# Performance work log

Hardware: AMD Instinct MI355X
Metric: run time of the kernel (lower is better)

## Reference

```python
import jax, jax.numpy as jnp
import numpy as np

# conv_ada hyperparameters from init_kwargs: ka=1, alpha=0.25, kw=0.2
KA1 = 1.0          # activation scale for conv1 (ka)
KA2 = 1.25         # activation scale for conv2 (ka + alpha)
KW = 0.2           # weight clipping threshold used by the binary weight STE


def ste_sign(x, clip=1.0):
    """Binary sign with straight-through estimator (hardtanh-style clip).
    Forward value is sign(x); gradient is that of clip(x, -clip, clip)."""
    xc = jnp.clip(x, -clip, clip)
    return xc + jax.lax.stop_gradient(jnp.sign(x) - xc)


def conv_bin(x, w, ka, kw):
    """1-bit activation / 1-bit weight 3x3 conv (conv_ada).
    Activations -> ka * sign(x); weights -> per-out-channel mean(|w|) * sign(w)."""
    xq = ka * ste_sign(x)
    alpha_w = jnp.mean(jnp.abs(w), axis=(1, 2, 3), keepdims=True)  # [O,1,1,1]
    wq = alpha_w * ste_sign(w, kw)
    return jax.lax.conv_general_dilated(
        xq, wq, window_strides=(1, 1), padding='SAME',
        dimension_numbers=('NCHW', 'OIHW', 'NCHW'))


def prelu(x, slope):
    # per-channel PReLU, slope shape [C]
    return jnp.where(x >= 0, x, slope[None, :, None, None] * x)


def pixel_shuffle(x, r=2):
    b, c, h, w = x.shape
    co = c // (r * r)
    x = x.reshape(b, co, r, r, h, w)
    x = x.transpose(0, 1, 4, 2, 5, 3)  # b, co, h, r, w, r
    return x.reshape(b, co, h * r, w * r)


def setup_inputs() -> dict:
    key = jax.random.key(0)
    ks = jax.random.split(key, 11)
    B, C, H, W = 8, 64, 256, 256
    return {
        'x': jax.random.normal(ks[0], (B, C, H, W), jnp.float32),
        'w1': jax.random.normal(ks[1], (C, C, 3, 3), jnp.float32) * 0.1,
        'w2': jax.random.normal(ks[2], (2 * C, C, 3, 3), jnp.float32) * 0.1,
        'b_in': jax.random.normal(ks[3], (1, C, 1, 1), jnp.float32) * 0.01,
        'b1': jax.random.normal(ks[4], (1, C, 1, 1), jnp.float32) * 0.01,
        's1': jax.random.uniform(ks[5], (C,), jnp.float32) * 0.25,
        'b2': jax.random.normal(ks[6], (1, C, 1, 1), jnp.float32) * 0.01,
        'b2_': jax.random.normal(ks[7], (1, C, 1, 1), jnp.float32) * 0.01,
        'b3': jax.random.normal(ks[8], (1, 2 * C, 1, 1), jnp.float32) * 0.01,
        's2': jax.random.uniform(ks[9], (2 * C,), jnp.float32) * 0.25,
        'b4': jax.random.normal(ks[10], (1, 2 * C, 1, 1), jnp.float32) * 0.01,
    }


def reference(x, w1, w2, b_in, b1, s1, b2, b2_, b3, s2, b4):
    out = conv_bin(x + b_in, w1, KA1, KW)       # move1_ -> conv1
    xres = out + x                              # residual x = out + x
    # NOTE: in the original forward, move1 -> prelu1 -> move2 are computed on
    # `out` and then immediately overwritten by out = move2_(x); that branch
    # is dead code and does not affect the output (b1, s1, b2 get zero grads).
    out = conv_bin(xres + b2_, w2, KA2, KW)     # move2_ -> conv2
    out = out + jnp.concatenate([xres, xres], axis=1)  # shortcut = cat(x, x)
    out = prelu(out + b3, s2) + b4              # move3 -> prelu2 -> move4
    return pixel_shuffle(out, 2)                # [B, C/2, 2H, 2W]
```

## Files before the change

kernel.cpp:

```cpp
#include <hip/hip_runtime.h>
#include <hip/hip_bf16.h>

typedef unsigned long long u64;
typedef unsigned int u32;
typedef unsigned short ushort8 __attribute__((ext_vector_type(8)));
typedef unsigned short ushortx16 __attribute__((ext_vector_type(16)));
typedef u64 u64x2 __attribute__((ext_vector_type(2)));
typedef u64 u64x4 __attribute__((ext_vector_type(4)));
typedef float fx2 __attribute__((ext_vector_type(2)));
typedef float fx4 __attribute__((ext_vector_type(4)));

#define IMG_H 256
#define IMG_W 256
#define CIN   64
#define HW    (IMG_H * IMG_W)
#define NPIX  (8 * HW)

static __device__ __forceinline__ float bf16bits_to_f32(unsigned short h) {
    union { u32 u; float f; } c;
    c.u = ((u32)h) << 16;
    return c.f;
}
static __device__ __forceinline__ unsigned short f32_to_bf16bits(float f) {
    __hip_bfloat16 hb = __float2bfloat16(f);
    return *(unsigned short*)&hb;
}

__global__ void prep_kernel(const float* __restrict__ w1,
                            const float* __restrict__ w2,
                            u64* __restrict__ w1b, float* __restrict__ a1,
                            u64* __restrict__ w2b, float* __restrict__ a2) {
    int blk = blockIdx.x;
    int lane = threadIdx.x;
    const float* w;
    u64* wb;
    float* al;
    if (blk < 64) { w = w1 + (size_t)blk * 576;        wb = w1b + blk * 9;        al = a1 + blk; }
    else          { w = w2 + (size_t)(blk - 64) * 576; wb = w2b + (blk - 64) * 9; al = a2 + (blk - 64); }

    const float* wi = w + lane * 9;
    float s = 0.f;
    u64 bits[9];
#pragma unroll
    for (int t = 0; t < 9; ++t) {
        float v = wi[t];
        s += fabsf(v);
        bits[t] = __ballot(v > 0.f);
    }
#pragma unroll
    for (int m = 32; m >= 1; m >>= 1) s += __shfl_xor(s, m);
    if (lane == 0) {
        *al = s * (1.f / 576.f);
#pragma unroll
        for (int t = 0; t < 9; ++t) wb[t] = bits[t];
    }
}

__global__ __launch_bounds__(256)
void pack_kernel(const float* __restrict__ x,
                 const float* __restrict__ b_in,
                 u64* __restrict__ bits1) {
    int tid = blockIdx.x * 256 + threadIdx.x;
    int n = tid >> 14;
    int p = (tid & 16383) * 4;
    const float* xp = x + (size_t)n * CIN * HW + p;
    u32 lo[4] = {0, 0, 0, 0}, hi[4] = {0, 0, 0, 0};
#pragma unroll
    for (int c = 0; c < 32; ++c) {
        fx4 v = *(const fx4*)(xp + (size_t)c * HW);
        float b = b_in[c];
#pragma unroll
        for (int q = 0; q < 4; ++q) lo[q] |= (u32)((v[q] + b) > 0.f) << c;
    }
#pragma unroll
    for (int c = 0; c < 32; ++c) {
        fx4 v = *(const fx4*)(xp + (size_t)(c + 32) * HW);
        float b = b_in[c + 32];
#pragma unroll
        for (int q = 0; q < 4; ++q) hi[q] |= (u32)((v[q] + b) > 0.f) << c;
    }
    u64x4 pk;
#pragma unroll
    for (int q = 0; q < 4; ++q) pk[q] = ((u64)hi[q] << 32) | lo[q];
    *(u64x4*)(bits1 + (size_t)n * HW + p) = pk;
}

__global__ __launch_bounds__(256)
void conv1_kernel(const float* __restrict__ x,
                  const float* __restrict__ b2_,
                  const u64* __restrict__ bits1,
                  const u64* __restrict__ wbits,
                  const float* __restrict__ alpha1,
                  ushort8* __restrict__ xres,
                  u64* __restrict__ bits2) {
    int i = blockIdx.x * 256 + threadIdx.x;
    int n = i >> 16, p = i & 65535;
    int y = p >> 8, xc = p & 255;

    u64 xb[9];
    int invmask = 0, nv = 0;
#pragma unroll
    for (int t = 0; t < 9; ++t) {
        int dy = t / 3 - 1, dx = t % 3 - 1;
        bool v = ((unsigned)(y + dy) < (unsigned)IMG_H) &
                 ((unsigned)(xc + dx) < (unsigned)IMG_W);
        xb[t] = v ? bits1[i + dy * IMG_W + dx] : 0ull;
        invmask |= (v ? 0 : 1) << t;
        nv += v ? 1 : 0;
    }

    const float* xp = x + (size_t)n * CIN * HW + p;
    u64 w2 = 0;

    float rvA[8], rvB[8];

    auto load_rv = [&](float* buf, int g) {
#pragma unroll
        for (int j = 0; j < 8; ++j)
            buf[j] = xp[(size_t)(g * 8 + j) * HW];
    };
    auto comp = [&](const float* buf, int g) {
        ushort8 pk;
        u32 gm = 0;
#pragma unroll
        for (int j = 0; j < 8; ++j) {
            int o = g * 8 + j;
            const u64* wo = wbits + o * 9;
            int D = 0;
#pragma unroll
            for (int t = 0; t < 9; ++t) D += __popcll(xb[t] ^ wo[t]);
            int S = 64 * nv - 2 * D;
            if (invmask) {
#pragma unroll
                for (int t = 0; t < 9; ++t)
                    if ((invmask >> t) & 1) S += 2 * __popcll(wo[t]);
            }
            float r = alpha1[o] * (float)S + buf[j];
            pk[j] = f32_to_bf16bits(r);
            gm |= (u32)((r + b2_[o]) > 0.f) << j;
        }
        xres[(size_t)(n * 8 + g) * HW + p] = pk;
        w2 |= (u64)gm << (8 * g);
    };

    load_rv(rvA, 0);
#pragma unroll 1
    for (int gg = 0; gg < 4; ++gg) {
        load_rv(rvB, 2 * gg + 1);
        comp(rvA, 2 * gg);
        if (gg < 3) load_rv(rvA, 2 * gg + 2);
        comp(rvB, 2 * gg + 1);
    }
    bits2[i] = w2;
}

__global__ __launch_bounds__(256)
void conv2_kernel(const ushort8* __restrict__ xres,
                  const u64* __restrict__ bits2,
                  const u64* __restrict__ wbits,
                  const float* __restrict__ alpha2,
                  const float* __restrict__ b3,
                  const float* __restrict__ s2,
                  const float* __restrict__ b4,
                  float* __restrict__ out) {
    int tid = blockIdx.x * 256 + threadIdx.x;
    int n = tid >> 15;
    int p = (tid & 32767) * 2;
    int y = p >> 8, xc = p & 255;

    u64 W[3][4];
    const u64* bp = bits2 + (size_t)n * HW;
#pragma unroll
    for (int r = 0; r < 3; ++r) {
        int yy = y - 1 + r;
        bool rv = (unsigned)yy < (unsigned)IMG_H;
        const u64* row = bp + yy * IMG_W + xc;
        W[r][0] = (rv && xc > 0)   ? row[-1] : 0ull;
        W[r][1] = rv ? row[0] : 0ull;
        W[r][2] = rv ? row[1] : 0ull;
        W[r][3] = (rv && xc < 254) ? row[2]  : 0ull;
    }
    int inv0 = 0, inv1 = 0, nv0 = 0, nv1 = 0;
#pragma unroll
    for (int t = 0; t < 9; ++t) {
        const int r = t / 3, c = t % 3;
        bool rv = (unsigned)(y - 1 + r) < (unsigned)IMG_H;
        bool v0 = rv && !(c == 0 && xc == 0);
        bool v1 = rv && !(c == 2 && xc == 254);
        inv0 |= (v0 ? 0 : 1) << t; nv0 += v0 ? 1 : 0;
        inv1 |= (v1 ? 0 : 1) << t; nv1 += v1 ? 1 : 0;
    }
    const int edge = inv0 | inv1;

    const ushortx16* xrp = (const ushortx16*)(xres + (size_t)n * 8 * HW + p);
    float* ob = out + (size_t)n * 32 * 512 * 512;
    const int Y = 2 * y, X = 2 * xc;

    ushortx16 xrA, xrB;

    auto comp = [&](const ushortx16& xr, int g) {
#pragma unroll
        for (int jj = 0; jj < 8; jj += 2) {
            float lo4[4], hi4[4];
#pragma unroll
            for (int q = 0; q < 2; ++q) {
                int o = g * 8 + jj + q;
                float xrv0 = bf16bits_to_f32(xr[jj + q]);
                float xrv1 = bf16bits_to_f32(xr[8 + jj + q]);
                {
                    const u64* wo = wbits + o * 9;
                    int D0 = 0, D1 = 0;
#pragma unroll
                    for (int t = 0; t < 9; ++t) {
                        const int r = t / 3, c = t % 3;
                        u64 w = wo[t];
                        D0 += __popcll(W[r][c] ^ w);
                        D1 += __popcll(W[r][c + 1] ^ w);
                    }
                    int S0 = 64 * nv0 - 2 * D0;
                    int S1 = 64 * nv1 - 2 * D1;
                    if (edge) {
#pragma unroll
                        for (int t = 0; t < 9; ++t) {
                            int pw = __popcll(wo[t]);
                            if ((inv0 >> t) & 1) S0 += 2 * pw;
                            if ((inv1 >> t) & 1) S1 += 2 * pw;
                        }
                    }
                    float ka = 1.25f * alpha2[o], bb = b3[o], ss = s2[o], b4v = b4[o];
                    float u0 = ka * (float)S0 + xrv0 + bb;
                    float u1 = ka * (float)S1 + xrv1 + bb;
                    u0 = (u0 >= 0.f) ? u0 : ss * u0;
                    u1 = (u1 >= 0.f) ? u1 : ss * u1;
                    lo4[q] = u0 + b4v;
                    lo4[2 + q] = u1 + b4v;
                }
                {
                    int o2 = o + 64;
                    const u64* wo = wbits + o2 * 9;
                    int D0 = 0, D1 = 0;
#pragma unroll
                    for (int t = 0; t < 9; ++t) {
                        const int r = t / 3, c = t % 3;
                        u64 w = wo[t];
                        D0 += __popcll(W[r][c] ^ w);
                        D1 += __popcll(W[r][c + 1] ^ w);
                    }
                    int S0 = 64 * nv0 - 2 * D0;
                    int S1 = 64 * nv1 - 2 * D1;
                    if (edge) {
#pragma unroll
                        for (int t = 0; t < 9; ++t) {
                            int pw = __popcll(wo[t]);
                            if ((inv0 >> t) & 1) S0 += 2 * pw;
                            if ((inv1 >> t) & 1) S1 += 2 * pw;
                        }
                    }
                    float ka = 1.25f * alpha2[o2], bb = b3[o2], ss = s2[o2], b4v = b4[o2];
                    float u0 = ka * (float)S0 + xrv0 + bb;
                    float u1 = ka * (float)S1 + xrv1 + bb;
                    u0 = (u0 >= 0.f) ? u0 : ss * u0;
                    u1 = (u1 >= 0.f) ? u1 : ss * u1;
                    hi4[q] = u0 + b4v;
                    hi4[2 + q] = u1 + b4v;
                }
            }
            int o = g * 8 + jj;
            int co = o >> 2;
            int r1 = (o >> 1) & 1;
            fx4 vl; vl.x = lo4[0]; vl.y = lo4[1]; vl.z = lo4[2]; vl.w = lo4[3];
            fx4 vh; vh.x = hi4[0]; vh.y = hi4[1]; vh.z = hi4[2]; vh.w = hi4[3];
            __builtin_nontemporal_store(
                vl, (fx4*)(ob + ((size_t)co * 512 + Y + r1) * 512 + X));
            __builtin_nontemporal_store(
                vh, (fx4*)(ob + ((size_t)(co + 16) * 512 + Y + r1) * 512 + X));
        }
    };

    xrA = xrp[0];
#pragma unroll 1
    for (int gg = 0; gg < 4; ++gg) {
        xrB = xrp[(size_t)(2 * gg + 1) * (HW / 2)];
        comp(xrA, 2 * gg);
        if (gg < 3) xrA = xrp[(size_t)(2 * gg + 2) * (HW / 2)];
        comp(xrB, 2 * gg + 1);
    }
}

extern "C" void kernel_launch(void* const* d_in, const int* in_sizes, int n_in,
                              void* d_out, int out_size, void* d_ws, size_t ws_size,
                              hipStream_t stream) {
    const float* x    = (const float*)d_in[0];
    const float* w1   = (const float*)d_in[1];
    const float* w2   = (const float*)d_in[2];
    const float* b_in = (const float*)d_in[3];
    const float* b2_  = (const float*)d_in[7];
    const float* b3   = (const float*)d_in[8];
    const float* s2   = (const float*)d_in[9];
    const float* b4   = (const float*)d_in[10];
    float* out = (float*)d_out;

    char* ws = (char*)d_ws;
    u64*   w1b   = (u64*)(ws + 0);
    u64*   w2b   = (u64*)(ws + 4608);
    float* a1    = (float*)(ws + 13824);
    float* a2    = (float*)(ws + 14080);
    u64*   bits1 = (u64*)(ws + 16384);
    u64*   bits2 = (u64*)(ws + 16384 + 4194304);
    ushort8* xres = (ushort8*)(ws + 16384 + 2 * 4194304);

    prep_kernel<<<192, 64, 0, stream>>>(w1, w2, w1b, a1, w2b, a2);

    pack_kernel <<<NPIX / 1024, 256, 0, stream>>>(x, b_in, bits1);
    conv1_kernel<<<NPIX / 256, 256, 0, stream>>>(x, b2_, bits1, w1b, a1, xres, bits2);
    conv2_kernel<<<NPIX / 512, 256, 0, stream>>>(xres, bits2, w2b, a2, b3, s2, b4, out);
}
```

Before: 204.6 us.

## Stage conv1 residual loads through LDS with async double-buffered global_load_lds

conv1 now reads the fp32 residual input for each 8-channel group with async global-to-LDS loads of 16 bytes per lane into a double-buffered shared tile. The next group is prefetched while the current one is computed, replacing per-thread strided register loads. The xres and bits2 outputs are written with nontemporal stores so they do not pollute the cache. The cost is a block barrier per group, and correctness relies on the async LDS writes having completed when the barrier is reached.

Result: slower. 211.4 us (+3.3%).

```diff
diff --git a/kernel.cpp b/kernel.cpp
--- a/kernel.cpp
+++ b/kernel.cpp
@@ -5,9 +5,7 @@
 typedef unsigned int u32;
 typedef unsigned short ushort8 __attribute__((ext_vector_type(8)));
 typedef unsigned short ushortx16 __attribute__((ext_vector_type(16)));
-typedef u64 u64x2 __attribute__((ext_vector_type(2)));
 typedef u64 u64x4 __attribute__((ext_vector_type(4)));
-typedef float fx2 __attribute__((ext_vector_type(2)));
 typedef float fx4 __attribute__((ext_vector_type(4)));
 
 #define IMG_H 256
@@ -93,9 +91,32 @@
                   const float* __restrict__ alpha1,
                   ushort8* __restrict__ xres,
                   u64* __restrict__ bits2) {
-    int i = blockIdx.x * 256 + threadIdx.x;
-    int n = i >> 16, p = i & 65535;
-    int y = p >> 8, xc = p & 255;
+    __shared__ float st[2][8][256];
+
+    const int tid = threadIdx.x;
+    const int blk = blockIdx.x;
+    const int i = blk * 256 + tid;
+    const int n = blk >> 8;
+    const int y = blk & 255;
+    const int p0 = y * IMG_W;
+    const int p = p0 + tid;
+    const int xc = tid;
+
+    const int wv = tid >> 6;
+    const int ln = tid & 63;
+    const float* xbase = x + (size_t)n * CIN * HW + p0;
+
+    auto stage = [&](int buf, int g) {
+#pragma unroll
+        for (int s = 0; s < 2; ++s) {
+            int cl = wv * 2 + s;
+            const float* gsrc = xbase + (size_t)(g * 8 + cl) * HW + ln * 4;
+            __builtin_amdgcn_global_load_lds(
+                (const __attribute__((address_space(1))) u32*)gsrc,
+                (__attribute__((address_space(3))) u32*)&st[buf][cl][0],
+                16, 0, 0);
+        }
+    };
 
     u64 xb[9];
     int invmask = 0, nv = 0;
@@ -109,17 +130,14 @@
         nv += v ? 1 : 0;
     }
 
-    const float* xp = x + (size_t)n * CIN * HW + p;
+    stage(0, 0);
+    __syncthreads();
+
     u64 w2 = 0;
-
-    float rvA[8], rvB[8];
-
-    auto load_rv = [&](float* buf, int g) {
-#pragma unroll
-        for (int j = 0; j < 8; ++j)
-            buf[j] = xp[(size_t)(g * 8 + j) * HW];
-    };
-    auto comp = [&](const float* buf, int g) {
+#pragma unroll 1
+    for (int g = 0; g < 8; ++g) {
+        if (g < 7) stage((g + 1) & 1, g + 1);
+
         ushort8 pk;
         u32 gm = 0;
 #pragma unroll
@@ -135,23 +153,15 @@
                 for (int t = 0; t < 9; ++t)
                     if ((invmask >> t) & 1) S += 2 * __popcll(wo[t]);
             }
-            float r = alpha1[o] * (float)S + buf[j];
+            float r = alpha1[o] * (float)S + st[g & 1][j][tid];
             pk[j] = f32_to_bf16bits(r);
             gm |= (u32)((r + b2_[o]) > 0.f) << j;
         }
-        xres[(size_t)(n * 8 + g) * HW + p] = pk;
+        __builtin_nontemporal_store(pk, xres + (size_t)(n * 8 + g) * HW + p);
         w2 |= (u64)gm << (8 * g);
-    };
-
-    load_rv(rvA, 0);
-#pragma unroll 1
-    for (int gg = 0; gg < 4; ++gg) {
-        load_rv(rvB, 2 * gg + 1);
-        comp(rvA, 2 * gg);
-        if (gg < 3) load_rv(rvA, 2 * gg + 2);
-        comp(rvB, 2 * gg + 1);
-    }
-    bits2[i] = w2;
+        __syncthreads();
+    }
+    __builtin_nontemporal_store(w2, bits2 + i);
 }
 
 __global__ __launch_bounds__(256)
```
